# Kernel tuning notes

Measured on AMD Instinct MI355X. Metric: run time of the kernel, lower is better.

## Reference

```python
import jax, jax.numpy as jnp
import numpy as np

NUM_GRAPHS = 64


def gcn_layer(h_in, W, b, src, dst, dinv, N):
    # h_in: [N, Fin]; W: [Fin, Fout]
    h = h_in @ W  # [N, Fout]
    norm = dinv[src] * dinv[dst]  # [E+N]
    msg = h[src] * norm[:, None]  # gather + scale, [E+N, Fout]
    out = jax.ops.segment_sum(msg, dst, num_segments=N)  # scatter-add
    return out + b


def setup_inputs() -> dict:
    key = jax.random.key(0)
    ks = jax.random.split(key, 12)
    N, E, Fin, H, C = 100000, 1600000, 256, 128, 2
    x = jax.random.normal(ks[0], (N, Fin), dtype=jnp.float32)
    edge_index = jax.random.randint(ks[1], (2, E), 0, N, dtype=jnp.int64)
    batch = jnp.sort(jax.random.randint(ks[2], (N,), 0, NUM_GRAPHS, dtype=jnp.int64))
    def glorot(k, fi, fo):
        s = (6.0 / (fi + fo)) ** 0.5
        return jax.random.uniform(k, (fi, fo), jnp.float32, -s, s)
    return {
        "x": x,
        "edge_index": edge_index,
        "batch": batch,
        "W1": glorot(ks[3], Fin, H), "b1": jnp.zeros((H,), jnp.float32),
        "W2": glorot(ks[4], H, H), "b2": jnp.zeros((H,), jnp.float32),
        "W3": glorot(ks[5], H, H), "b3": jnp.zeros((H,), jnp.float32),
        "Wc": glorot(ks[6], H, C), "bc": jnp.zeros((C,), jnp.float32),
    }


def reference(x, edge_index, batch, W1, b1, W2, b2, W3, b3, Wc, bc):
    N = x.shape[0]
    # add self-loops once (shared across layers, as GCNConv does per call)
    loops = jnp.arange(N, dtype=edge_index.dtype)
    src = jnp.concatenate([edge_index[0], loops])
    dst = jnp.concatenate([edge_index[1], loops])
    # symmetric normalization: deg over targets of A+I
    deg = jax.ops.segment_sum(jnp.ones_like(dst, dtype=x.dtype), dst, num_segments=N)
    dinv = jax.lax.rsqrt(deg)  # deg >= 1 due to self-loops

    h = jax.nn.relu(gcn_layer(x, W1, b1, src, dst, dinv, N))
    h = jax.nn.relu(gcn_layer(h, W2, b2, src, dst, dinv, N))
    h = gcn_layer(h, W3, b3, src, dst, dinv, N)

    # global mean pool per graph
    sums = jax.ops.segment_sum(h, batch, num_segments=NUM_GRAPHS)
    cnts = jax.ops.segment_sum(jnp.ones((N,), h.dtype), batch, num_segments=NUM_GRAPHS)
    pooled = sums / jnp.maximum(cnts, 1.0)[:, None]
    return pooled @ Wc + bc
```

## Files before the change

### kernel.cpp

```cpp
#include <hip/hip_runtime.h>
#include <hip/hip_bf16.h>


typedef unsigned int uint;
typedef unsigned short ushort;
typedef __bf16 bf16x8 __attribute__((ext_vector_type(8)));
typedef float f32x4 __attribute__((ext_vector_type(4)));

__device__ inline uint bf16rne(float x) {
  uint u = __float_as_uint(x);
  return (u + 0x7FFFu + ((u >> 16) & 1u)) >> 16;
}
__device__ inline uint packbf(float a, float b) {
  return bf16rne(a) | (bf16rne(b) << 16);
}
__device__ inline float bflo(uint v) { return __uint_as_float(v << 16); }
__device__ inline float bfhi(uint v) { return __uint_as_float(v & 0xFFFF0000u); }

__global__ __launch_bounds__(256) void init_degf(float* degf, int N) {
  int i = blockIdx.x * 256 + threadIdx.x;
  if (i < N) degf[i] = 1.0f;
}

__global__ __launch_bounds__(256) void deg_count(const int* __restrict__ dstIdx,
                                                 float* degf, int E) {
  int e = blockIdx.x * 256 + threadIdx.x;
  if (e < E) atomicAdd(&degf[dstIdx[e]], 1.0f);
}

__global__ __launch_bounds__(256) void dinv_k(const float* __restrict__ degf,
                                              float* __restrict__ dinv, int N) {
  int i = blockIdx.x * 256 + threadIdx.x;
  if (i < N) dinv[i] = rsqrtf(degf[i]);
}

__global__ __launch_bounds__(256) void scan_local(const float* __restrict__ degf,
                                                  int* __restrict__ offsets,
                                                  int* __restrict__ blockSums, int N) {
  __shared__ int lds[256];
  int t = threadIdx.x;
  int base = blockIdx.x * 1024 + t * 4;
  int c[4], s = 0;
#pragma unroll
  for (int i = 0; i < 4; i++) {
    int idx = base + i;
    c[i] = (idx < N) ? ((int)degf[idx] - 1) : 0;
    s += c[i];
  }
  lds[t] = s;
  __syncthreads();
  for (int d = 1; d < 256; d <<= 1) {
    int add = (t >= d) ? lds[t - d] : 0;
    __syncthreads();
    lds[t] += add;
    __syncthreads();
  }
  int incl = lds[t];
  int run = incl - s;
#pragma unroll
  for (int i = 0; i < 4; i++) {
    int idx = base + i;
    if (idx < N) offsets[idx] = run;
    run += c[i];
  }
  if (t == 255) blockSums[blockIdx.x] = incl;
}

__global__ __launch_bounds__(128) void scan_block(const int* __restrict__ blockSums,
                                                  int* __restrict__ blockOff, int nb) {
  __shared__ int lds[128];
  int t = threadIdx.x;
  int v = (t < nb) ? blockSums[t] : 0;
  lds[t] = v;
  __syncthreads();
  for (int d = 1; d < 128; d <<= 1) {
    int add = (t >= d) ? lds[t - d] : 0;
    __syncthreads();
    lds[t] += add;
    __syncthreads();
  }
  blockOff[t] = lds[t] - v;
}

__global__ __launch_bounds__(256) void scan_add(int* __restrict__ offsets,
                                                const int* __restrict__ blockOff, int N) {
  int i = blockIdx.x * 256 + threadIdx.x;
  if (i < N) offsets[i] += blockOff[i >> 10];
}

__global__ __launch_bounds__(256) void fill_csr(const int* __restrict__ ei,
                                                const float* __restrict__ dinv,
                                                const int* __restrict__ offsets,
                                                int* __restrict__ cursor,
                                                int2* __restrict__ csr, int E) {
  int e = blockIdx.x * 256 + threadIdx.x;
  if (e < E) {
    int s = ei[e];
    int d = ei[E + e];
    int pos = offsets[d] + atomicAdd(&cursor[d], 1);
    csr[pos] = make_int2(s, __float_as_int(dinv[s]));
  }
}

__global__ __launch_bounds__(256) void wt_k(const float* __restrict__ W,
                                            ushort* __restrict__ WT, int K) {
  int idx = blockIdx.x * 256 + threadIdx.x;
  if (idx >= K * 128) return;
  int k = idx >> 7, c = idx & 127;
  WT[c * K + k] = (ushort)bf16rne(W[idx]);
}

template <int K, bool AF32>
__global__ __launch_bounds__(128) void mgemm_k(const void* __restrict__ Ain,
                                               const ushort* __restrict__ WT,
                                               ushort* __restrict__ C, int N) {
  constexpr int KT = K / 32;
  int t = threadIdx.x;
  int wv = t >> 6, l = t & 63;
  int row16 = blockIdx.x * 32 + wv * 16;
  size_t rA = (size_t)(row16 + (l & 15)) * K;
  int koff = (l >> 4) * 8;

  bf16x8 a[KT];
  if (AF32) {
    const float* A = (const float*)Ain;
#pragma unroll
    for (int kt = 0; kt < KT; kt++) {
      const float4* p = (const float4*)(A + rA + kt * 32 + koff);
      float4 lo = p[0], hi = p[1];
      bf16x8 av;
      av[0] = (__bf16)lo.x; av[1] = (__bf16)lo.y; av[2] = (__bf16)lo.z; av[3] = (__bf16)lo.w;
      av[4] = (__bf16)hi.x; av[5] = (__bf16)hi.y; av[6] = (__bf16)hi.z; av[7] = (__bf16)hi.w;
      a[kt] = av;
    }
  } else {
    const ushort* A = (const ushort*)Ain;
#pragma unroll
    for (int kt = 0; kt < KT; kt++) a[kt] = *(const bf16x8*)(A + rA + kt * 32 + koff);
  }

  f32x4 acc[8];
#pragma unroll
  for (int ct = 0; ct < 8; ct++) { f32x4 z = {0.f, 0.f, 0.f, 0.f}; acc[ct] = z; }

  const ushort* WTl = WT + (size_t)(l & 15) * K + koff;
#pragma unroll
  for (int kt = 0; kt < KT; kt++) {
#pragma unroll
    for (int ct = 0; ct < 8; ct++) {
      bf16x8 b = *(const bf16x8*)(WTl + (size_t)ct * 16 * K + kt * 32);
      acc[ct] = __builtin_amdgcn_mfma_f32_16x16x32_bf16(a[kt], b, acc[ct], 0, 0, 0);
    }
  }

  int rowD = row16 + (l >> 4) * 4;
  int colD = l & 15;
  __bf16* Cb = (__bf16*)C;
#pragma unroll
  for (int ct = 0; ct < 8; ct++) {
#pragma unroll
    for (int r = 0; r < 4; r++) {
      Cb[(size_t)(rowD + r) * 128 + ct * 16 + colD] = (__bf16)acc[ct][r];
    }
  }
}

template <bool RELU, bool OUTBF>
__global__ __launch_bounds__(256) void agg_k(const ushort* __restrict__ T,
                                             const float* __restrict__ dinv,
                                             const int2* __restrict__ csr,
                                             const int* __restrict__ offsets,
                                             const float* __restrict__ degf,
                                             const float* __restrict__ bias,
                                             void* __restrict__ Hout, int N) {
  int w = threadIdx.x >> 6, l = threadIdx.x & 63;
  int n = blockIdx.x * 4 + w;
  if (n >= N) return;
  float di = dinv[n];
  int off = offsets[n];
  int cnt = (int)degf[n] - 1;
  const uint* Tn = (const uint*)(T + (size_t)n * 128);
  uint selfv = Tn[l];
  float a0 = 0.0f, a1 = 0.0f;

  for (int j0 = 0; j0 < cnt; j0 += 64) {
    int idx = j0 + l;
    int2 e = (idx < cnt) ? csr[off + idx] : make_int2(0, 0);
    int ex = e.x;
    float ew = __int_as_float(e.y);
    int m = min(cnt - j0, 64);
    int j = 0;
    for (; j + 4 <= m; j += 4) {
      int r0 = __shfl(ex, j), r1 = __shfl(ex, j + 1);
      int r2 = __shfl(ex, j + 2), r3 = __shfl(ex, j + 3);
      float w0 = __shfl(ew, j), w1 = __shfl(ew, j + 1);
      float w2 = __shfl(ew, j + 2), w3 = __shfl(ew, j + 3);
      uint v0 = ((const uint*)(T + (size_t)r0 * 128))[l];
      uint v1 = ((const uint*)(T + (size_t)r1 * 128))[l];
      uint v2 = ((const uint*)(T + (size_t)r2 * 128))[l];
      uint v3 = ((const uint*)(T + (size_t)r3 * 128))[l];
      a0 = fmaf(w0, bflo(v0), a0); a1 = fmaf(w0, bfhi(v0), a1);
      a0 = fmaf(w1, bflo(v1), a0); a1 = fmaf(w1, bfhi(v1), a1);
      a0 = fmaf(w2, bflo(v2), a0); a1 = fmaf(w2, bfhi(v2), a1);
      a0 = fmaf(w3, bflo(v3), a0); a1 = fmaf(w3, bfhi(v3), a1);
    }
    for (; j < m; j++) {
      int r = __shfl(ex, j);
      float wj = __shfl(ew, j);
      uint v = ((const uint*)(T + (size_t)r * 128))[l];
      a0 = fmaf(wj, bflo(v), a0);
      a1 = fmaf(wj, bfhi(v), a1);
    }
  }

  float2 b = ((const float2*)bias)[l];
  float o0 = di * a0 + di * di * bflo(selfv) + b.x;
  float o1 = di * a1 + di * di * bfhi(selfv) + b.y;
  if (RELU) { o0 = fmaxf(o0, 0.0f); o1 = fmaxf(o1, 0.0f); }
  if (OUTBF) {
    ((uint*)Hout)[(size_t)n * 64 + l] = packbf(o0, o1);
  } else {
    ((float2*)Hout)[(size_t)n * 64 + l] = make_float2(o0, o1);
  }
}

__global__ __launch_bounds__(256) void boundary_k(const int* __restrict__ batch,
                                                  int* __restrict__ gstart,
                                                  int* __restrict__ gend, int N) {
  int i = blockIdx.x * 256 + threadIdx.x;
  if (i >= N) return;
  int b = batch[i];
  if (i == 0 || batch[i - 1] != b) gstart[b] = i;
  if (i == N - 1 || batch[i + 1] != b) gend[b] = i + 1;
}

__global__ __launch_bounds__(128) void pool_k(const float* __restrict__ H,
                                              const int* __restrict__ gstart,
                                              const int* __restrict__ gend,
                                              float* __restrict__ sums) {
  int g = blockIdx.x >> 3, s = blockIdx.x & 7;
  int gs = gstart[g], ge = gend[g];
  int len = ge - gs;
  if (len <= 0) return;
  int chunk = (len + 7) >> 3;
  int r0 = gs + s * chunk;
  int r1 = min(r0 + chunk, ge);
  if (r0 >= r1) return;
  int f = threadIdx.x;
  float local = 0.0f;
  int r = r0;
  for (; r + 4 <= r1; r += 4) {
    float h0 = H[(size_t)r * 128 + f];
    float h1 = H[(size_t)(r + 1) * 128 + f];
    float h2 = H[(size_t)(r + 2) * 128 + f];
    float h3 = H[(size_t)(r + 3) * 128 + f];
    local += (h0 + h1) + (h2 + h3);
  }
  for (; r < r1; r++) local += H[(size_t)r * 128 + f];
  atomicAdd(&sums[g * 128 + f], local);
}

__global__ __launch_bounds__(128) void final_k(const float* __restrict__ sums,
                                               const int* __restrict__ gstart,
                                               const int* __restrict__ gend,
                                               const float* __restrict__ Wc,
                                               const float* __restrict__ bc,
                                               float* __restrict__ out) {
  int t = threadIdx.x;
  int g = t >> 1, c = t & 1;
  float cg = fmaxf((float)(gend[g] - gstart[g]), 1.0f);
  float acc = bc[c];
  for (int f = 0; f < 128; f++) acc += (sums[g * 128 + f] / cg) * Wc[f * 2 + c];
  out[g * 2 + c] = acc;
}

extern "C" void kernel_launch(void* const* d_in, const int* in_sizes, int n_in,
                              void* d_out, int out_size, void* d_ws, size_t ws_size,
                              hipStream_t stream) {
  const float* x = (const float*)d_in[0];
  const int* ei = (const int*)d_in[1];
  const int* batch = (const int*)d_in[2];
  const float* W1 = (const float*)d_in[3];
  const float* b1 = (const float*)d_in[4];
  const float* W2 = (const float*)d_in[5];
  const float* b2 = (const float*)d_in[6];
  const float* W3 = (const float*)d_in[7];
  const float* b3 = (const float*)d_in[8];
  const float* Wc = (const float*)d_in[9];
  const float* bc = (const float*)d_in[10];
  float* out = (float*)d_out;

  int N = in_sizes[0] / 256;
  int E = in_sizes[1] / 2;

  char* ws = (char*)d_ws;
  size_t off = 0;
  auto alloc = [&](size_t bytes) -> void* {
    off = (off + 255) & ~(size_t)255;
    void* p = ws + off;
    off += bytes;
    return p;
  };
  float* degf = (float*)alloc((size_t)N * 4);
  float* dinv = (float*)alloc((size_t)N * 4);
  int* offsets = (int*)alloc((size_t)N * 4);
  int* cursor = (int*)alloc((size_t)N * 4);
  int* blockSums = (int*)alloc(256 * 4);
  int* blockOff = (int*)alloc(256 * 4);
  float* sums = (float*)alloc(64 * 128 * 4);
  int* gstart = (int*)alloc(64 * 4);
  int* gend = (int*)alloc(64 * 4);
  ushort* WT1 = (ushort*)alloc(256 * 128 * 2);
  ushort* WT2 = (ushort*)alloc(128 * 128 * 2);
  ushort* WT3 = (ushort*)alloc(128 * 128 * 2);
  int2* csr = (int2*)alloc((size_t)E * 8);
  ushort* bufT = (ushort*)alloc((size_t)N * 128 * 2);
  ushort* bufHb = (ushort*)alloc((size_t)N * 128 * 2);
  float* bufH = (float*)alloc((size_t)N * 128 * 4);

  int gN = (N + 255) / 256;
  int gE = (E + 255) / 256;
  int nb = (N + 1023) / 1024;

  hipMemsetAsync(cursor, 0, (size_t)N * 4, stream);
  hipMemsetAsync(sums, 0, 64 * 128 * 4, stream);
  hipMemsetAsync(gstart, 0, 64 * 4, stream);
  hipMemsetAsync(gend, 0, 64 * 4, stream);

  init_degf<<<gN, 256, 0, stream>>>(degf, N);
  deg_count<<<gE, 256, 0, stream>>>(ei + E, degf, E);
  dinv_k<<<gN, 256, 0, stream>>>(degf, dinv, N);

  scan_local<<<nb, 256, 0, stream>>>(degf, offsets, blockSums, N);
  scan_block<<<1, 128, 0, stream>>>(blockSums, blockOff, nb);
  scan_add<<<gN, 256, 0, stream>>>(offsets, blockOff, N);
  fill_csr<<<gE, 256, 0, stream>>>(ei, dinv, offsets, cursor, csr, E);

  boundary_k<<<gN, 256, 0, stream>>>(batch, gstart, gend, N);
  wt_k<<<(256 * 128 + 255) / 256, 256, 0, stream>>>(W1, WT1, 256);
  wt_k<<<(128 * 128 + 255) / 256, 256, 0, stream>>>(W2, WT2, 128);
  wt_k<<<(128 * 128 + 255) / 256, 256, 0, stream>>>(W3, WT3, 128);

  mgemm_k<256, true><<<N / 32, 128, 0, stream>>>(x, WT1, bufT, N);
  agg_k<true, true><<<(N + 3) / 4, 256, 0, stream>>>(bufT, dinv, csr, offsets, degf, b1, bufHb, N);
  mgemm_k<128, false><<<N / 32, 128, 0, stream>>>(bufHb, WT2, bufT, N);
  agg_k<true, true><<<(N + 3) / 4, 256, 0, stream>>>(bufT, dinv, csr, offsets, degf, b2, bufHb, N);
  mgemm_k<128, false><<<N / 32, 128, 0, stream>>>(bufHb, WT3, bufT, N);
  agg_k<false, false><<<(N + 3) / 4, 256, 0, stream>>>(bufT, dinv, csr, offsets, degf, b3, bufH, N);

  pool_k<<<64 * 8, 128, 0, stream>>>(bufH, gstart, gend, sums);
  final_k<<<1, 128, 0, stream>>>(sums, gstart, gend, Wc, bc, out);
}
```

Baseline: 693.1 us.

## Stage pre-swizzled weights in LDS and compute two row tiles per wave in GEMM

The transposed weight matrix is reordered on the device into the exact MFMA fragment order and copied into shared memory once per block. Each wave now computes two 16-row tiles that share each B fragment, and blocks cover 128 rows with 256 threads, which cuts global reads of weights per output row. The CSR fill seeds its cursor from a device copy of the offsets, so each edge needs one atomic instead of an extra offsets load. The costs are a 64KB LDS footprint for K=256, which can limit occupancy, and higher register pressure from the doubled accumulators.

```diff
diff --git a/kernel.cpp b/kernel.cpp
--- a/kernel.cpp
+++ b/kernel.cpp
@@ -90,77 +90,105 @@
 
 __global__ __launch_bounds__(256) void fill_csr(const int* __restrict__ ei,
                                                 const float* __restrict__ dinv,
-                                                const int* __restrict__ offsets,
                                                 int* __restrict__ cursor,
                                                 int2* __restrict__ csr, int E) {
   int e = blockIdx.x * 256 + threadIdx.x;
   if (e < E) {
     int s = ei[e];
     int d = ei[E + e];
-    int pos = offsets[d] + atomicAdd(&cursor[d], 1);
+    int pos = atomicAdd(&cursor[d], 1);
     csr[pos] = make_int2(s, __float_as_int(dinv[s]));
   }
 }
 
-__global__ __launch_bounds__(256) void wt_k(const float* __restrict__ W,
-                                            ushort* __restrict__ WT, int K) {
+__global__ __launch_bounds__(256) void wtp_k(const float* __restrict__ W,
+                                             ushort* __restrict__ WTp, int K, int KT) {
   int idx = blockIdx.x * 256 + threadIdx.x;
   if (idx >= K * 128) return;
-  int k = idx >> 7, c = idx & 127;
-  WT[c * K + k] = (ushort)bf16rne(W[idx]);
+  int j = idx & 7;
+  int l = (idx >> 3) & 63;
+  int f = idx >> 9;
+  int kt = f % KT, ct = f / KT;
+  int k = kt * 32 + (l >> 4) * 8 + j;
+  int c = ct * 16 + (l & 15);
+  WTp[idx] = (ushort)bf16rne(W[k * 128 + c]);
 }
 
 template <int K, bool AF32>
-__global__ __launch_bounds__(128) void mgemm_k(const void* __restrict__ Ain,
-                                               const ushort* __restrict__ WT,
+__global__ __launch_bounds__(256) void mgemm_k(const void* __restrict__ Ain,
+                                               const ushort* __restrict__ WTp,
                                                ushort* __restrict__ C, int N) {
   constexpr int KT = K / 32;
+  __shared__ ushort bs[K * 128];
+
   int t = threadIdx.x;
+  {
+    const uint4* src = (const uint4*)WTp;
+    uint4* dst = (uint4*)bs;
+    const int NCHUNK = K * 128 / 8;
+#pragma unroll
+    for (int i = t; i < NCHUNK; i += 256) dst[i] = src[i];
+  }
+
   int wv = t >> 6, l = t & 63;
-  int row16 = blockIdx.x * 32 + wv * 16;
-  size_t rA = (size_t)(row16 + (l & 15)) * K;
+  int rowBase = blockIdx.x * 128 + wv * 32;
   int koff = (l >> 4) * 8;
 
-  bf16x8 a[KT];
-  if (AF32) {
-    const float* A = (const float*)Ain;
+  bf16x8 a[2][KT];
+#pragma unroll
+  for (int m = 0; m < 2; m++) {
+    int row = rowBase + m * 16 + (l & 15);
+    row = min(row, N - 1);
+    if (AF32) {
+      const float* A = (const float*)Ain;
+      const float* Ar = A + (size_t)row * K;
+#pragma unroll
+      for (int kt = 0; kt < KT; kt++) {
+        const float4* p = (const float4*)(Ar + kt * 32 + koff);
+        float4 lo = p[0], hi = p[1];
+        bf16x8 av;
+        av[0] = (__bf16)lo.x; av[1] = (__bf16)lo.y; av[2] = (__bf16)lo.z; av[3] = (__bf16)lo.w;
+        av[4] = (__bf16)hi.x; av[5] = (__bf16)hi.y; av[6] = (__bf16)hi.z; av[7] = (__bf16)hi.w;
+        a[m][kt] = av;
+      }
+    } else {
+      const ushort* A = (const ushort*)Ain;
+      const ushort* Ar = A + (size_t)row * K;
+#pragma unroll
+      for (int kt = 0; kt < KT; kt++) a[m][kt] = *(const bf16x8*)(Ar + kt * 32 + koff);
+    }
+  }
+
+  f32x4 acc[2][8];
+#pragma unroll
+  for (int m = 0; m < 2; m++)
+#pragma unroll
+    for (int ct = 0; ct < 8; ct++) { f32x4 z = {0.f, 0.f, 0.f, 0.f}; acc[m][ct] = z; }
+
+  __syncthreads();
+
+#pragma unroll
+  for (int ct = 0; ct < 8; ct++) {
 #pragma unroll
     for (int kt = 0; kt < KT; kt++) {
-      const float4* p = (const float4*)(A + rA + kt * 32 + koff);
-      float4 lo = p[0], hi = p[1];
-      bf16x8 av;
-      av[0] = (__bf16)lo.x; av[1] = (__bf16)lo.y; av[2] = (__bf16)lo.z; av[3] = (__bf16)lo.w;
-      av[4] = (__bf16)hi.x; av[5] = (__bf16)hi.y; av[6] = (__bf16)hi.z; av[7] = (__bf16)hi.w;
-      a[kt] = av;
-    }
-  } else {
-    const ushort* A = (const ushort*)Ain;
-#pragma unroll
-    for (int kt = 0; kt < KT; kt++) a[kt] = *(const bf16x8*)(A + rA + kt * 32 + koff);
-  }
-
-  f32x4 acc[8];
-#pragma unroll
-  for (int ct = 0; ct < 8; ct++) { f32x4 z = {0.f, 0.f, 0.f, 0.f}; acc[ct] = z; }
-
-  const ushort* WTl = WT + (size_t)(l & 15) * K + koff;
-#pragma unroll
-  for (int kt = 0; kt < KT; kt++) {
-#pragma unroll
-    for (int ct = 0; ct < 8; ct++) {
-      bf16x8 b = *(const bf16x8*)(WTl + (size_t)ct * 16 * K + kt * 32);
-      acc[ct] = __builtin_amdgcn_mfma_f32_16x16x32_bf16(a[kt], b, acc[ct], 0, 0, 0);
-    }
-  }
-
-  int rowD = row16 + (l >> 4) * 4;
+      bf16x8 b = *(const bf16x8*)&bs[(size_t)((ct * KT + kt) * 64 + l) * 8];
+      acc[0][ct] = __builtin_amdgcn_mfma_f32_16x16x32_bf16(a[0][kt], b, acc[0][ct], 0, 0, 0);
+      acc[1][ct] = __builtin_amdgcn_mfma_f32_16x16x32_bf16(a[1][kt], b, acc[1][ct], 0, 0, 0);
+    }
+  }
+
   int colD = l & 15;
   __bf16* Cb = (__bf16*)C;
 #pragma unroll
-  for (int ct = 0; ct < 8; ct++) {
-#pragma unroll
-    for (int r = 0; r < 4; r++) {
-      Cb[(size_t)(rowD + r) * 128 + ct * 16 + colD] = (__bf16)acc[ct][r];
+  for (int m = 0; m < 2; m++) {
+    int rowD = rowBase + m * 16 + (l >> 4) * 4;
+#pragma unroll
+    for (int ct = 0; ct < 8; ct++) {
+#pragma unroll
+      for (int r = 0; r < 4; r++) {
+        int row = rowD + r;
+        if (row < N) Cb[(size_t)row * 128 + ct * 16 + colD] = (__bf16)acc[m][ct][r];
+      }
     }
   }
 }
@@ -310,9 +338,9 @@
   float* sums = (float*)alloc(64 * 128 * 4);
   int* gstart = (int*)alloc(64 * 4);
   int* gend = (int*)alloc(64 * 4);
-  ushort* WT1 = (ushort*)alloc(256 * 128 * 2);
-  ushort* WT2 = (ushort*)alloc(128 * 128 * 2);
-  ushort* WT3 = (ushort*)alloc(128 * 128 * 2);
+  ushort* WTp1 = (ushort*)alloc(256 * 128 * 2);
+  ushort* WTp2 = (ushort*)alloc(128 * 128 * 2);
+  ushort* WTp3 = (ushort*)alloc(128 * 128 * 2);
   int2* csr = (int2*)alloc((size_t)E * 8);
   ushort* bufT = (ushort*)alloc((size_t)N * 128 * 2);
   ushort* bufHb = (ushort*)alloc((size_t)N * 128 * 2);
@@ -321,8 +349,8 @@
   int gN = (N + 255) / 256;
   int gE = (E + 255) / 256;
   int nb = (N + 1023) / 1024;
-
-  hipMemsetAsync(cursor, 0, (size_t)N * 4, stream);
+  int nblk = (N + 127) / 128;
+
   hipMemsetAsync(sums, 0, 64 * 128 * 4, stream);
   hipMemsetAsync(gstart, 0, 64 * 4, stream);
   hipMemsetAsync(gend, 0, 64 * 4, stream);
@@ -334,18 +362,19 @@
   scan_local<<<nb, 256, 0, stream>>>(degf, offsets, blockSums, N);
   scan_block<<<1, 128, 0, stream>>>(blockSums, blockOff, nb);
   scan_add<<<gN, 256, 0, stream>>>(offsets, blockOff, N);
-  fill_csr<<<gE, 256, 0, stream>>>(ei, dinv, offsets, cursor, csr, E);
+  hipMemcpyAsync(cursor, offsets, (size_t)N * 4, hipMemcpyDeviceToDevice, stream);
+  fill_csr<<<gE, 256, 0, stream>>>(ei, dinv, cursor, csr, E);
 
   boundary_k<<<gN, 256, 0, stream>>>(batch, gstart, gend, N);
-  wt_k<<<(256 * 128 + 255) / 256, 256, 0, stream>>>(W1, WT1, 256);
-  wt_k<<<(128 * 128 + 255) / 256, 256, 0, stream>>>(W2, WT2, 128);
-  wt_k<<<(128 * 128 + 255) / 256, 256, 0, stream>>>(W3, WT3, 128);
-
-  mgemm_k<256, true><<<N / 32, 128, 0, stream>>>(x, WT1, bufT, N);
+  wtp_k<<<(256 * 128 + 255) / 256, 256, 0, stream>>>(W1, WTp1, 256, 8);
+  wtp_k<<<(128 * 128 + 255) / 256, 256, 0, stream>>>(W2, WTp2, 128, 4);
+  wtp_k<<<(128 * 128 + 255) / 256, 256, 0, stream>>>(W3, WTp3, 128, 4);
+
+  mgemm_k<256, true><<<nblk, 256, 0, stream>>>(x, WTp1, bufT, N);
   agg_k<true, true><<<(N + 3) / 4, 256, 0, stream>>>(bufT, dinv, csr, offsets, degf, b1, bufHb, N);
-  mgemm_k<128, false><<<N / 32, 128, 0, stream>>>(bufHb, WT2, bufT, N);
+  mgemm_k<128, false><<<nblk, 256, 0, stream>>>(bufHb, WTp2, bufT, N);
   agg_k<true, true><<<(N + 3) / 4, 256, 0, stream>>>(bufT, dinv, csr, offsets, degf, b2, bufHb, N);
-  mgemm_k<128, false><<<N / 32, 128, 0, stream>>>(bufHb, WT3, bufT, N);
+  mgemm_k<128, false><<<nblk, 256, 0, stream>>>(bufHb, WTp3, bufT, N);
   agg_k<false, false><<<(N + 3) / 4, 256, 0, stream>>>(bufT, dinv, csr, offsets, degf, b3, bufH, N);
 
   pool_k<<<64 * 8, 128, 0, stream>>>(bufH, gstart, gend, sums);
```

Result: faster. 638.9 us (-7.8%).
